# Optimization experiments

Hardware: AMD Instinct MI355X
Metric: run time of the kernel (lower is better)

The kernel has to match this reference:

```python
import jax, jax.numpy as jnp
import numpy as np

ENT_TOTAL = 100000
REL_TOTAL = 1000
ENT_SIZE = 200
REL_SIZE = 200
BATCH = 16384
MARGIN = 4.0


def setup_inputs() -> dict:
    key = jax.random.key(0)
    ks = jax.random.split(key, 8)
    return {
        "pos_h": jax.random.randint(ks[0], (BATCH,), 0, ENT_TOTAL, dtype=jnp.int32),
        "pos_t": jax.random.randint(ks[1], (BATCH,), 0, ENT_TOTAL, dtype=jnp.int32),
        "pos_r": jax.random.randint(ks[2], (BATCH,), 0, REL_TOTAL, dtype=jnp.int32),
        "neg_h": jax.random.randint(ks[3], (BATCH,), 0, ENT_TOTAL, dtype=jnp.int32),
        "neg_t": jax.random.randint(ks[4], (BATCH,), 0, ENT_TOTAL, dtype=jnp.int32),
        "ent_emb": jax.random.normal(ks[5], (ENT_TOTAL, ENT_SIZE), dtype=jnp.float32) * 0.1,
        "rel_emb": jax.random.normal(ks[6], (REL_TOTAL, REL_SIZE), dtype=jnp.float32) * 0.1,
        "transfer": jax.random.normal(ks[7], (REL_TOTAL, ENT_SIZE * REL_SIZE), dtype=jnp.float32) * 0.05,
    }


def _l2norm(x):
    # tf.nn.l2_normalize semantics: x / sqrt(max(sum(x^2), eps))
    return x * jax.lax.rsqrt(jnp.maximum(jnp.sum(x * x, axis=-1, keepdims=True), 1e-12))


def _calc(h, t, r):
    return jnp.abs(_l2norm(h) + _l2norm(r) - _l2norm(t))


def reference(pos_h, pos_t, pos_r, neg_h, neg_t, ent_emb, rel_emb, transfer):
    # gather embeddings
    pos_h_e = ent_emb[pos_h]                 # [b, ent]
    pos_t_e = ent_emb[pos_t]
    pos_r_e = rel_emb[pos_r]                 # [b, rel]
    neg_h_e = ent_emb[neg_h]
    neg_t_e = ent_emb[neg_t]
    # relation-specific transfer matrices [b, ent, rel]
    pos_mat = transfer[pos_r].reshape(-1, ENT_SIZE, REL_SIZE)
    # project entities into relation space: [b, ent] x [b, ent, rel] -> [b, rel]
    p_h = jnp.einsum('be,ber->br', pos_h_e, pos_mat)
    p_t = jnp.einsum('be,ber->br', pos_t_e, pos_mat)
    n_h = jnp.einsum('be,ber->br', neg_h_e, pos_mat)  # negative_rel == 0: reuse pos matrix
    n_t = jnp.einsum('be,ber->br', neg_t_e, pos_mat)
    p_score = jnp.sum(_calc(p_h, p_t, pos_r_e), axis=-1, keepdims=True)  # [b,1]
    n_score = jnp.sum(_calc(n_h, n_t, pos_r_e), axis=-1, keepdims=True)
    loss = jnp.mean(jnp.maximum(p_score - n_score + MARGIN, 0.0))
    return loss
```

## Files before the change

kernel.cpp:

```cpp
#include <hip/hip_runtime.h>

#define ENT 200
#define RELD 200
#define NREL 1000
#define NBATCH 16384
#define MARGIN 4.0f
#define CHUNK 32
#define NVEC 128
#define MAXCHUNKS 1512

#define NSLOT 416
#define BSTRIDE_I 419
#define BBUF 1676

#define WS_NCHUNKS 3072
#define WS_CHUNKS 3076
#define WS_LIST 11268
#define WS_ELEM 27652

typedef __attribute__((ext_vector_type(8))) short short8;
typedef __attribute__((ext_vector_type(4))) float floatx4;

__device__ __forceinline__ unsigned short f2bf(float x) {
    unsigned u = __float_as_uint(x);
    u = (u + 0x7FFFu + ((u >> 16) & 1u)) >> 16;
    return (unsigned short)u;
}

__device__ __forceinline__ float wave_reduce(float v) {
#pragma unroll
    for (int off = 32; off > 0; off >>= 1) v += __shfl_down(v, off, 64);
    return v;
}

__global__ __launch_bounds__(1024) void prep_kernel(const int* __restrict__ pos_r,
                                                    int* __restrict__ ws) {
    __shared__ int cnt_s[NREL];
    __shared__ int off_s[NREL];
    __shared__ int scan_s[1024];
    const int tid = threadIdx.x;

    for (int i = tid; i < NREL; i += 1024) cnt_s[i] = 0;
    __syncthreads();

    int rl[16];
#pragma unroll
    for (int k = 0; k < 16; ++k) {
        rl[k] = pos_r[(k << 10) + tid];
        atomicAdd(&cnt_s[rl[k]], 1);
    }
    __syncthreads();

    const int cnt = (tid < NREL) ? cnt_s[tid] : 0;

    scan_s[tid] = cnt;
    __syncthreads();
#pragma unroll
    for (int off = 1; off < 1024; off <<= 1) {
        const int add = (tid >= off) ? scan_s[tid - off] : 0;
        __syncthreads();
        scan_s[tid] += add;
        __syncthreads();
    }
    const int myoff = scan_s[tid] - cnt;
    if (tid < NREL) off_s[tid] = myoff;
    __syncthreads();

    const int nch = (cnt + CHUNK - 1) / CHUNK;
    scan_s[tid] = nch;
    __syncthreads();
#pragma unroll
    for (int off = 1; off < 1024; off <<= 1) {
        const int add = (tid >= off) ? scan_s[tid - off] : 0;
        __syncthreads();
        scan_s[tid] += add;
        __syncthreads();
    }
    const int cbase = scan_s[tid] - nch;
    int4* chunks = (int4*)(ws + WS_CHUNKS);
    for (int k = 0; k < nch; ++k)
        chunks[cbase + k] = make_int4(tid, myoff + CHUNK * k, min(CHUNK, cnt - CHUNK * k), 0);
    if (tid == 1023) ws[WS_NCHUNKS] = scan_s[1023];

    if (tid < NREL) cnt_s[tid] = 0;
    __syncthreads();
#pragma unroll
    for (int k = 0; k < 16; ++k) {
        const int r = rl[k];
        const int p = off_s[r] + atomicAdd(&cnt_s[r], 1);
        ws[WS_LIST + p] = (k << 10) + tid;
    }
}

__global__ __launch_bounds__(512) void transr_mfma_kernel(
    const int* __restrict__ pos_h, const int* __restrict__ pos_t,
    const int* __restrict__ neg_h, const int* __restrict__ neg_t,
    const float* __restrict__ ent_emb, const float* __restrict__ rel_emb,
    const float* __restrict__ transfer, int* __restrict__ ws)
{
    const int nch = ws[WS_NCHUNKS];
    const int stride = (nch + 7) >> 3;
    const int bidx = blockIdx.x;
    if ((bidx >> 3) >= stride) return;
    const int cix = (bidx & 7) * stride + (bidx >> 3);
    if (cix >= nch) return;

    __shared__ short sB[2 * BBUF * 8];
    __shared__ int items_s[CHUNK];
    __shared__ int rows[NVEC];

    const int4 ck = ((const int4*)(ws + WS_CHUNKS))[cix];
    const int r = ck.x, start = ck.y, cnt = ck.z;

    const int tid  = threadIdx.x;
    const int lane = tid & 63;
    const int wv   = tid >> 6;
    const int q    = lane >> 4;
    const int n    = lane & 15;
    const bool wactive = (wv * 4 < cnt);

    if (tid < CHUNK) items_s[tid] = ws[WS_LIST + start + min(tid, cnt - 1)];
    __syncthreads();
    if (tid < NVEC) {
        const int b = items_s[tid >> 2];
        const int c = tid & 3;
        rows[tid] = (c == 0) ? pos_h[b] : (c == 1) ? pos_t[b] : (c == 2) ? neg_h[b] : neg_t[b];
    }
    __syncthreads();

    short8 afrag[7];
#pragma unroll
    for (int s = 0; s < 7; ++s) afrag[s] = (short8){0, 0, 0, 0, 0, 0, 0, 0};
    if (wactive) {
        const int row = rows[wv * 16 + n];
        const float* __restrict__ ab = ent_emb + (size_t)row * ENT;
#pragma unroll
        for (int s = 0; s < 7; ++s) {
            const int e0 = s * 32 + q * 8;
            if (e0 < ENT) {
                float v[8];
                *(float4*)(&v[0]) = *(const float4*)(ab + e0);
                *(float4*)(&v[4]) = *(const float4*)(ab + e0 + 4);
                short8 f;
#pragma unroll
                for (int j = 0; j < 8; ++j) f[j] = (short)f2bf(v[j]);
                afrag[s] = f;
            }
        }
    }

    const int slot = tid;
    const int sq   = slot / 52;
    const int srem = slot - sq * 52;
    const int scol = srem * 4;
    const bool sact = (slot < NSLOT) && (scol < RELD);
    const float* __restrict__ Mb = transfer + (size_t)r * (ENT * RELD) + scol;
    const int k0 = sq * 8;

    float fm[8][4];
    short8 bh[4];
#define LOAD_SLAB(p_)                                                          \
    {                                                                          \
        const int kk = (p_) * 64 + k0;                                         \
        if (sact && kk < ENT) {                                                \
            _Pragma("unroll")                                                  \
            for (int j = 0; j < 8; ++j)                                        \
                *(float4*)(&fm[j][0]) = *(const float4*)(Mb + (size_t)(kk + j) * RELD); \
        } else {                                                               \
            _Pragma("unroll")                                                  \
            for (int j = 0; j < 8; ++j) {                                      \
                fm[j][0] = 0.f; fm[j][1] = 0.f; fm[j][2] = 0.f; fm[j][3] = 0.f;\
            }                                                                  \
        }                                                                      \
    }
#define CONV_SLAB()                                                            \
    {                                                                          \
        _Pragma("unroll")                                                      \
        for (int i = 0; i < 4; ++i) {                                          \
            short8 f;                                                          \
            _Pragma("unroll")                                                  \
            for (int j = 0; j < 8; ++j) f[j] = (short)f2bf(fm[j][i]);          \
            bh[i] = f;                                                         \
        }                                                                      \
    }
#define WRITE_SLAB(buf_)                                                       \
    if (slot < NSLOT) {                                                        \
        _Pragma("unroll")                                                      \
        for (int i = 0; i < 4; ++i)                                            \
            *(short8*)(&sB[((buf_) * BBUF + i * BSTRIDE_I + slot) * 8]) = bh[i]; \
    }

    floatx4 acc[13];
#pragma unroll
    for (int c = 0; c < 13; ++c) acc[c] = (floatx4){0.f, 0.f, 0.f, 0.f};

    const int rb16 = (n & 3) * BSTRIDE_I + q * 52 + (n >> 2);

    LOAD_SLAB(0); CONV_SLAB(); WRITE_SLAB(0);
    LOAD_SLAB(1); CONV_SLAB();
    __syncthreads();

#pragma unroll
    for (int p = 0; p < 4; ++p) {
        if (p < 2) LOAD_SLAB(p + 2);
        if (wactive) {
            const int bb = (p & 1) * BBUF;
#pragma unroll
            for (int ks = 0; ks < 2; ++ks) {
                if (p * 64 + ks * 32 < ENT) {
#pragma unroll
                    for (int c = 0; c < 13; ++c) {
                        const short8 bf = *(const short8*)(&sB[(bb + rb16 + ks * 208 + c * 4) * 8]);
                        acc[c] = __builtin_amdgcn_mfma_f32_16x16x32_bf16(afrag[2 * p + ks], bf, acc[c], 0, 0, 0);
                    }
                }
            }
        }
        if (p < 3) WRITE_SLAB((p + 1) & 1);
        if (p < 2) CONV_SLAB();
        if (p < 3) __syncthreads();
    }

    if (wactive) {
        float rl[13];
        const float* __restrict__ rb = rel_emb + (size_t)r * RELD;
#pragma unroll
        for (int c = 0; c < 13; ++c) {
            const int col = c * 16 + n;
            rl[c] = (col < RELD) ? rb[col] : 0.f;
        }
        float nsq[4] = {0.f, 0.f, 0.f, 0.f};
        float rsq = 0.f;
#pragma unroll
        for (int c = 0; c < 13; ++c) {
            nsq[0] += acc[c][0] * acc[c][0];
            nsq[1] += acc[c][1] * acc[c][1];
            nsq[2] += acc[c][2] * acc[c][2];
            nsq[3] += acc[c][3] * acc[c][3];
            rsq += rl[c] * rl[c];
        }
#pragma unroll
        for (int m = 1; m < 16; m <<= 1) {
#pragma unroll
            for (int k = 0; k < 4; ++k) nsq[k] += __shfl_xor(nsq[k], m, 64);
            rsq += __shfl_xor(rsq, m, 64);
        }
        float inv[4];
#pragma unroll
        for (int k = 0; k < 4; ++k) inv[k] = rsqrtf(fmaxf(nsq[k], 1e-12f));
        const float invr = rsqrtf(fmaxf(rsq, 1e-12f));

        float psum = 0.f, nsum = 0.f;
#pragma unroll
        for (int c = 0; c < 13; ++c) {
            const float rr = rl[c] * invr;
            psum += fabsf(acc[c][0] * inv[0] + rr - acc[c][1] * inv[1]);
            nsum += fabsf(acc[c][2] * inv[2] + rr - acc[c][3] * inv[3]);
        }
#pragma unroll
        for (int m = 1; m < 16; m <<= 1) {
            psum += __shfl_xor(psum, m, 64);
            nsum += __shfl_xor(nsum, m, 64);
        }
        const int item = wv * 4 + q;
        if (n == 0 && item < cnt) {
            float* elem = (float*)(ws + WS_ELEM);
            elem[items_s[item]] = fmaxf(psum - nsum + MARGIN, 0.f);
        }
    }
}

__global__ __launch_bounds__(256) void reduce_mean_kernel(const int* __restrict__ ws,
                                                          float* __restrict__ out) {
    __shared__ float sred[4];
    const float4* elem = (const float4*)(ws + WS_ELEM);
    float s = 0.f;
    for (int i = threadIdx.x; i < NBATCH / 4; i += 256) {
        const float4 v = elem[i];
        s += v.x + v.y + v.z + v.w;
    }
    s = wave_reduce(s);
    const int lane = threadIdx.x & 63;
    const int wvv = threadIdx.x >> 6;
    if (lane == 0) sred[wvv] = s;
    __syncthreads();
    if (threadIdx.x == 0)
        out[0] = (sred[0] + sred[1] + sred[2] + sred[3]) * (1.0f / (float)NBATCH);
}

extern "C" void kernel_launch(void* const* d_in, const int* in_sizes, int n_in,
                              void* d_out, int out_size, void* d_ws, size_t ws_size,
                              hipStream_t stream) {
    const int* pos_h = (const int*)d_in[0];
    const int* pos_t = (const int*)d_in[1];
    const int* pos_r = (const int*)d_in[2];
    const int* neg_h = (const int*)d_in[3];
    const int* neg_t = (const int*)d_in[4];
    const float* ent_emb = (const float*)d_in[5];
    const float* rel_emb = (const float*)d_in[6];
    const float* transfer = (const float*)d_in[7];

    int* ws = (int*)d_ws;
    float* out = (float*)d_out;

    prep_kernel<<<1, 1024, 0, stream>>>(pos_r, ws);
    transr_mfma_kernel<<<MAXCHUNKS, 512, 0, stream>>>(
        pos_h, pos_t, neg_h, neg_t, ent_emb, rel_emb, transfer, ws);
    reduce_mean_kernel<<<1, 256, 0, stream>>>(ws, out);
}
```

Baseline: 319.2 us.

## Pre-gather and bf16-convert entity rows into workspace before the MFMA kernel

Adds a separate kernel that gathers the four entity rows per batch item from ent_emb, converts them to bf16 and writes them, padded, into a contiguous workspace buffer. The main MFMA kernel then loads its A fragments directly from that buffer, which removes the index indirection, the extra syncthreads and the in-kernel float-to-bf16 conversion. The aim is to take the random-access gather latency off the critical path of the transfer-matrix kernel. The cost is an extra launch and a round trip of about 58 MB through workspace. The old kernel is kept as a fallback for when the workspace is too small.

```diff
diff --git a/kernel.cpp b/kernel.cpp
--- a/kernel.cpp
+++ b/kernel.cpp
@@ -17,6 +17,10 @@
 #define WS_CHUNKS 3076
 #define WS_LIST 11268
 #define WS_ELEM 27652
+#define WS_A_BYTE 262144
+#define NROWS (NBATCH * 4)
+#define A_ROW_SLOTS 28
+#define WS_NEEDED (WS_A_BYTE + (size_t)NROWS * A_ROW_SLOTS * 16)
 
 typedef __attribute__((ext_vector_type(8))) short short8;
 typedef __attribute__((ext_vector_type(4))) float floatx4;
@@ -92,11 +96,33 @@
     }
 }
 
-__global__ __launch_bounds__(512) void transr_mfma_kernel(
+__global__ __launch_bounds__(256) void agather_kernel(
     const int* __restrict__ pos_h, const int* __restrict__ pos_t,
     const int* __restrict__ neg_h, const int* __restrict__ neg_t,
-    const float* __restrict__ ent_emb, const float* __restrict__ rel_emb,
-    const float* __restrict__ transfer, int* __restrict__ ws)
+    const float* __restrict__ ent_emb, int* __restrict__ ws)
+{
+    short8* __restrict__ A = (short8*)((char*)ws + WS_A_BYTE);
+    const int unit = threadIdx.x >> 5;
+    const int j = threadIdx.x & 31;
+    for (int R = blockIdx.x * 8 + unit; R < NROWS; R += gridDim.x * 8) {
+        const int b = R >> 2, c = R & 3;
+        const int idx = (c == 0) ? pos_h[b] : (c == 1) ? pos_t[b] : (c == 2) ? neg_h[b] : neg_t[b];
+        short8 f = {0, 0, 0, 0, 0, 0, 0, 0};
+        if (j < 25) {
+            const float* __restrict__ src = ent_emb + (size_t)idx * ENT + j * 8;
+            float v[8];
+            *(float4*)(&v[0]) = *(const float4*)(src);
+            *(float4*)(&v[4]) = *(const float4*)(src + 4);
+#pragma unroll
+            for (int k = 0; k < 8; ++k) f[k] = (short)f2bf(v[k]);
+        }
+        if (j < A_ROW_SLOTS) A[(size_t)R * A_ROW_SLOTS + j] = f;
+    }
+}
+
+__global__ __launch_bounds__(512) void transr_mfma_kernel(
+    const float* __restrict__ rel_emb, const float* __restrict__ transfer,
+    int* __restrict__ ws)
 {
     const int nch = ws[WS_NCHUNKS];
     const int stride = (nch + 7) >> 3;
@@ -107,7 +133,6 @@
 
     __shared__ short sB[2 * BBUF * 8];
     __shared__ int items_s[CHUNK];
-    __shared__ int rows[NVEC];
 
     const int4 ck = ((const int4*)(ws + WS_CHUNKS))[cix];
     const int r = ck.x, start = ck.y, cnt = ck.z;
@@ -121,32 +146,16 @@
 
     if (tid < CHUNK) items_s[tid] = ws[WS_LIST + start + min(tid, cnt - 1)];
     __syncthreads();
-    if (tid < NVEC) {
-        const int b = items_s[tid >> 2];
-        const int c = tid & 3;
-        rows[tid] = (c == 0) ? pos_h[b] : (c == 1) ? pos_t[b] : (c == 2) ? neg_h[b] : neg_t[b];
-    }
-    __syncthreads();
 
     short8 afrag[7];
 #pragma unroll
     for (int s = 0; s < 7; ++s) afrag[s] = (short8){0, 0, 0, 0, 0, 0, 0, 0};
     if (wactive) {
-        const int row = rows[wv * 16 + n];
-        const float* __restrict__ ab = ent_emb + (size_t)row * ENT;
-#pragma unroll
-        for (int s = 0; s < 7; ++s) {
-            const int e0 = s * 32 + q * 8;
-            if (e0 < ENT) {
-                float v[8];
-                *(float4*)(&v[0]) = *(const float4*)(ab + e0);
-                *(float4*)(&v[4]) = *(const float4*)(ab + e0 + 4);
-                short8 f;
-#pragma unroll
-                for (int j = 0; j < 8; ++j) f[j] = (short)f2bf(v[j]);
-                afrag[s] = f;
-            }
-        }
+        const int R = items_s[wv * 4 + (n >> 2)] * 4 + (n & 3);
+        const short8* __restrict__ ap =
+            (const short8*)((const char*)ws + WS_A_BYTE) + (size_t)R * A_ROW_SLOTS + q;
+#pragma unroll
+        for (int s = 0; s < 7; ++s) afrag[s] = ap[s * 4];
     }
 
     const int slot = tid;
@@ -270,6 +279,154 @@
     }
 }
 
+__global__ __launch_bounds__(512) void transr_mfma_fb_kernel(
+    const int* __restrict__ pos_h, const int* __restrict__ pos_t,
+    const int* __restrict__ neg_h, const int* __restrict__ neg_t,
+    const float* __restrict__ ent_emb, const float* __restrict__ rel_emb,
+    const float* __restrict__ transfer, int* __restrict__ ws)
+{
+    const int nch = ws[WS_NCHUNKS];
+    const int stride = (nch + 7) >> 3;
+    const int bidx = blockIdx.x;
+    if ((bidx >> 3) >= stride) return;
+    const int cix = (bidx & 7) * stride + (bidx >> 3);
+    if (cix >= nch) return;
+
+    __shared__ short sB[2 * BBUF * 8];
+    __shared__ int items_s[CHUNK];
+    __shared__ int rows[NVEC];
+
+    const int4 ck = ((const int4*)(ws + WS_CHUNKS))[cix];
+    const int r = ck.x, start = ck.y, cnt = ck.z;
+
+    const int tid  = threadIdx.x;
+    const int lane = tid & 63;
+    const int wv   = tid >> 6;
+    const int q    = lane >> 4;
+    const int n    = lane & 15;
+    const bool wactive = (wv * 4 < cnt);
+
+    if (tid < CHUNK) items_s[tid] = ws[WS_LIST + start + min(tid, cnt - 1)];
+    __syncthreads();
+    if (tid < NVEC) {
+        const int b = items_s[tid >> 2];
+        const int c = tid & 3;
+        rows[tid] = (c == 0) ? pos_h[b] : (c == 1) ? pos_t[b] : (c == 2) ? neg_h[b] : neg_t[b];
+    }
+    __syncthreads();
+
+    short8 afrag[7];
+#pragma unroll
+    for (int s = 0; s < 7; ++s) afrag[s] = (short8){0, 0, 0, 0, 0, 0, 0, 0};
+    if (wactive) {
+        const int row = rows[wv * 16 + n];
+        const float* __restrict__ ab = ent_emb + (size_t)row * ENT;
+#pragma unroll
+        for (int s = 0; s < 7; ++s) {
+            const int e0 = s * 32 + q * 8;
+            if (e0 < ENT) {
+                float v[8];
+                *(float4*)(&v[0]) = *(const float4*)(ab + e0);
+                *(float4*)(&v[4]) = *(const float4*)(ab + e0 + 4);
+                short8 f;
+#pragma unroll
+                for (int j = 0; j < 8; ++j) f[j] = (short)f2bf(v[j]);
+                afrag[s] = f;
+            }
+        }
+    }
+
+    const int slot = tid;
+    const int sq   = slot / 52;
+    const int srem = slot - sq * 52;
+    const int scol = srem * 4;
+    const bool sact = (slot < NSLOT) && (scol < RELD);
+    const float* __restrict__ Mb = transfer + (size_t)r * (ENT * RELD) + scol;
+    const int k0 = sq * 8;
+
+    float fm[8][4];
+    short8 bh[4];
+
+    floatx4 acc[13];
+#pragma unroll
+    for (int c = 0; c < 13; ++c) acc[c] = (floatx4){0.f, 0.f, 0.f, 0.f};
+
+    const int rb16 = (n & 3) * BSTRIDE_I + q * 52 + (n >> 2);
+
+    LOAD_SLAB(0); CONV_SLAB(); WRITE_SLAB(0);
+    LOAD_SLAB(1); CONV_SLAB();
+    __syncthreads();
+
+#pragma unroll
+    for (int p = 0; p < 4; ++p) {
+        if (p < 2) LOAD_SLAB(p + 2);
+        if (wactive) {
+            const int bb = (p & 1) * BBUF;
+#pragma unroll
+            for (int ks = 0; ks < 2; ++ks) {
+                if (p * 64 + ks * 32 < ENT) {
+#pragma unroll
+                    for (int c = 0; c < 13; ++c) {
+                        const short8 bf = *(const short8*)(&sB[(bb + rb16 + ks * 208 + c * 4) * 8]);
+                        acc[c] = __builtin_amdgcn_mfma_f32_16x16x32_bf16(afrag[2 * p + ks], bf, acc[c], 0, 0, 0);
+                    }
+                }
+            }
+        }
+        if (p < 3) WRITE_SLAB((p + 1) & 1);
+        if (p < 2) CONV_SLAB();
+        if (p < 3) __syncthreads();
+    }
+
+    if (wactive) {
+        float rl[13];
+        const float* __restrict__ rb = rel_emb + (size_t)r * RELD;
+#pragma unroll
+        for (int c = 0; c < 13; ++c) {
+            const int col = c * 16 + n;
+            rl[c] = (col < RELD) ? rb[col] : 0.f;
+        }
+        float nsq[4] = {0.f, 0.f, 0.f, 0.f};
+        float rsq = 0.f;
+#pragma unroll
+        for (int c = 0; c < 13; ++c) {
+            nsq[0] += acc[c][0] * acc[c][0];
+            nsq[1] += acc[c][1] * acc[c][1];
+            nsq[2] += acc[c][2] * acc[c][2];
+            nsq[3] += acc[c][3] * acc[c][3];
+            rsq += rl[c] * rl[c];
+        }
+#pragma unroll
+        for (int m = 1; m < 16; m <<= 1) {
+#pragma unroll
+            for (int k = 0; k < 4; ++k) nsq[k] += __shfl_xor(nsq[k], m, 64);
+            rsq += __shfl_xor(rsq, m, 64);
+        }
+        float inv[4];
+#pragma unroll
+        for (int k = 0; k < 4; ++k) inv[k] = rsqrtf(fmaxf(nsq[k], 1e-12f));
+        const float invr = rsqrtf(fmaxf(rsq, 1e-12f));
+
+        float psum = 0.f, nsum = 0.f;
+#pragma unroll
+        for (int c = 0; c < 13; ++c) {
+            const float rr = rl[c] * invr;
+            psum += fabsf(acc[c][0] * inv[0] + rr - acc[c][1] * inv[1]);
+            nsum += fabsf(acc[c][2] * inv[2] + rr - acc[c][3] * inv[3]);
+        }
+#pragma unroll
+        for (int m = 1; m < 16; m <<= 1) {
+            psum += __shfl_xor(psum, m, 64);
+            nsum += __shfl_xor(nsum, m, 64);
+        }
+        const int item = wv * 4 + q;
+        if (n == 0 && item < cnt) {
+            float* elem = (float*)(ws + WS_ELEM);
+            elem[items_s[item]] = fmaxf(psum - nsum + MARGIN, 0.f);
+        }
+    }
+}
+
 __global__ __launch_bounds__(256) void reduce_mean_kernel(const int* __restrict__ ws,
                                                           float* __restrict__ out) {
     __shared__ float sred[4];
@@ -304,7 +461,12 @@
     float* out = (float*)d_out;
 
     prep_kernel<<<1, 1024, 0, stream>>>(pos_r, ws);
-    transr_mfma_kernel<<<MAXCHUNKS, 512, 0, stream>>>(
-        pos_h, pos_t, neg_h, neg_t, ent_emb, rel_emb, transfer, ws);
+    if (ws_size >= WS_NEEDED) {
+        agather_kernel<<<2048, 256, 0, stream>>>(pos_h, pos_t, neg_h, neg_t, ent_emb, ws);
+        transr_mfma_kernel<<<MAXCHUNKS, 512, 0, stream>>>(rel_emb, transfer, ws);
+    } else {
+        transr_mfma_fb_kernel<<<MAXCHUNKS, 512, 0, stream>>>(
+            pos_h, pos_t, neg_h, neg_t, ent_emb, rel_emb, transfer, ws);
+    }
     reduce_mean_kernel<<<1, 256, 0, stream>>>(ws, out);
 }
```

Result: no change. 325.0 us (+1.8%).
